# Kernel tuning notes

Hardware: AMD Instinct MI355X
Metric: run time of the kernel (lower is better)

The kernel has to match this reference:

```python
import jax, jax.numpy as jnp
import numpy as np


def setup_inputs() -> dict:
    key = jax.random.key(0)
    k0, k1, k2, k3 = jax.random.split(key, 4)
    B, H, W, C = 2, 128, 128, 512
    N_SPIX = 256  # (H/8)*(W/8) superpixels on an 8-px grid
    x = jax.random.normal(k0, (B, H, W, C), jnp.float32)
    sims = jax.random.uniform(k1, (B, H, W, 9), jnp.float32)
    sinds = jax.random.randint(k2, (B, H, W, 9), 0, N_SPIX, jnp.int32)
    W_qk = jax.random.normal(k3, (C, 2 * C), jnp.float32) * 0.02
    b_qk = jnp.zeros((2 * C,), jnp.float32)
    return {"x": x, "sims": sims, "sinds": sinds, "W_qk": W_qk, "b_qk": b_qk,
            "kernel_size": 7, "num_heads": 4}


def reference(x, sims, sinds, W_qk, b_qk, kernel_size, num_heads):
    """Soft-neighborhood superpixel attention scores.

    attn[b,g,si,h,w,ki] = <q[b,g,h,w], k[b,g,hj,wj]> + log p_j(s)
    where (hj,wj) is the ki-th pixel of the clamped (NATTEN-style) KxK window
    around (h,w), s = sinds[b,h,w,si] is the si-th neighboring-superpixel id
    of pixel (h,w), and p_j(s) = sum_m sims[b,hj,wj,m] * [sinds[b,hj,wj,m]==s]
    (the soft probability that key pixel j belongs to superpixel s; entries
    where s is not among j's 9 neighbor superpixels stay at -inf, matching
    the -inf-initialized attn buffer of the CUDA kernel).
    """
    B, H, W, C = x.shape
    K = kernel_size
    hd = C // num_heads
    r = K // 2

    # qk projection -> (B, heads, H, W, hd) for q and k (permute(3,0,4,1,2,5))
    qk = (x @ W_qk + b_qk).reshape(B, H, W, 2, num_heads, hd)
    q = jnp.moveaxis(qk[:, :, :, 0], 3, 1)  # (B,HD,H,W,hd)
    k = jnp.moveaxis(qk[:, :, :, 1], 3, 1)

    # NATTEN clamped window starts
    hs = jnp.clip(jnp.arange(H) - r, 0, H - K)  # (H,)
    ws = jnp.clip(jnp.arange(W) - r, 0, W - K)  # (W,)
    s_i = sinds  # (B,H,W,9): superpixel ids of pixel i's 9 neighbors

    dots, logps = [], []
    for dh in range(K):
        hj = hs + dh  # (H,)
        for dw in range(K):
            wj = ws + dw  # (W,)
            # gather key/sims/sinds at window offset (dh,dw)
            k_off = k[:, :, hj[:, None], wj[None, :], :]        # (B,HD,H,W,hd)
            dots.append(jnp.einsum('bghwf,bghwf->bghw', q, k_off))
            sind_j = sinds[:, hj[:, None], wj[None, :], :]      # (B,H,W,9)
            sim_j = sims[:, hj[:, None], wj[None, :], :]        # (B,H,W,9)
            # p_j(s_i): match i's si-th superpixel against j's 9 ids
            match = sind_j[:, :, :, None, :] == s_i[:, :, :, :, None]  # (B,H,W,9si,9m)
            pj = jnp.sum(jnp.where(match, sim_j[:, :, :, None, :], 0.0), axis=-1)  # (B,H,W,9)
            logps.append(jnp.where(pj > 0, jnp.log(jnp.maximum(pj, 1e-30)), -jnp.inf))

    dots = jnp.stack(dots, axis=-1)            # (B,HD,H,W,K*K)
    logp = jnp.stack(logps, axis=-1)           # (B,H,W,9,K*K)
    logp = jnp.moveaxis(logp, 3, 1)            # (B,9,H,W,K*K)
    attn = dots[:, :, None] + logp[:, None]    # (B,HD,9,H,W,K*K)
    return attn
```

## Files before the change

kernel.cpp:

```cpp
#include <hip/hip_runtime.h>
#include <hip/hip_bf16.h>
#include <math.h>

#define BATCH 2
#define HH 128
#define WW 128
#define CC 512
#define NH 4
#define HD 128
#define KS 7
#define RR 3
#define KK2 49
#define NSI 9

#define GM (BATCH*HH*WW)
#define GK CC
#define GN (2*CC)

#define NEG_HUGE (-1.0e30f)

typedef __attribute__((ext_vector_type(8))) short bf16x8;
typedef __attribute__((ext_vector_type(4))) float f32x4;

__device__ __forceinline__ float sout(float v) {
    return fminf(fmaxf(v, -3.0e38f), 3.0e38f);
}
__device__ __forceinline__ float bflo(unsigned int u) {
    return __builtin_bit_cast(float, u << 16);
}
__device__ __forceinline__ float bfhi(unsigned int u) {
    return __builtin_bit_cast(float, u & 0xffff0000u);
}
__device__ __forceinline__ unsigned short f2bf(float f) {
    unsigned int u = __builtin_bit_cast(unsigned int, f);
    u += 0x7fffu + ((u >> 16) & 1u);
    return (unsigned short)(u >> 16);
}

__device__ __forceinline__ void gl_lds16(const unsigned short* g, unsigned short* l) {
    __builtin_amdgcn_global_load_lds(
        (const __attribute__((address_space(1))) unsigned int*)g,
        (__attribute__((address_space(3))) unsigned int*)l, 16, 0, 0);
}

__global__ __launch_bounds__(256) void xcast(const float* __restrict__ x,
                                             unsigned short* __restrict__ xb) {
    int t = blockIdx.x * 256 + threadIdx.x;
    const float4* s = (const float4*)(x + (size_t)t * 8);
    float4 v0 = s[0], v1 = s[1];
    bf16x8 pk;
    pk[0] = (short)f2bf(v0.x); pk[1] = (short)f2bf(v0.y);
    pk[2] = (short)f2bf(v0.z); pk[3] = (short)f2bf(v0.w);
    pk[4] = (short)f2bf(v1.x); pk[5] = (short)f2bf(v1.y);
    pk[6] = (short)f2bf(v1.z); pk[7] = (short)f2bf(v1.w);
    *(bf16x8*)(xb + (size_t)t * 8) = pk;
}

__global__ __launch_bounds__(256) void wtrans(const float* __restrict__ W,
                                              unsigned short* __restrict__ Wt) {
    int t = blockIdx.x * 256 + threadIdx.x;
    int n = t >> 9, k = t & 511;
    Wt[(size_t)n * GK + k] = f2bf(W[(size_t)k * GN + n]);
}

#define TBM 128
#define TBN 128
#define TBK 64

__global__ __launch_bounds__(256, 3) void qk_gemm_async(
        const unsigned short* __restrict__ xb,
        const unsigned short* __restrict__ Wt,
        const float* __restrict__ bias,
        unsigned short* __restrict__ Cout)
{
    __shared__ unsigned short As[TBM * TBK];
    __shared__ unsigned short Bs[TBN * TBK];

    const int n0 = blockIdx.x * TBN;
    const int m0 = blockIdx.y * TBM;
    const int tid = threadIdx.x;
    const int lane = tid & 63;
    const int wid = tid >> 6;
    const int wr = wid >> 1, wc = wid & 1;

    f32x4 acc[4][4];
#pragma unroll
    for (int i = 0; i < 4; ++i)
#pragma unroll
        for (int j = 0; j < 4; ++j) acc[i][j] = (f32x4){0.f, 0.f, 0.f, 0.f};

    const int srow = lane >> 3;
    const int scol = (lane & 7) * 8;

    for (int k0 = 0; k0 < GK; k0 += TBK) {
#pragma unroll
        for (int i = 0; i < 4; ++i) {
            int chunk = wid * 4 + i;
            int row = chunk * 8 + srow;
            gl_lds16(xb + (size_t)(m0 + row) * GK + k0 + scol, &As[chunk * 512]);
            gl_lds16(Wt + (size_t)(n0 + row) * GK + k0 + scol, &Bs[chunk * 512]);
        }
        __syncthreads();

#pragma unroll
        for (int ks = 0; ks < 2; ++ks) {
            const int koff = ks * 32 + (lane >> 4) * 8;
            bf16x8 af[4], bfr[4];
#pragma unroll
            for (int i = 0; i < 4; ++i)
                af[i] = *(const bf16x8*)&As[(wr * 64 + i * 16 + (lane & 15)) * TBK + koff];
#pragma unroll
            for (int j = 0; j < 4; ++j)
                bfr[j] = *(const bf16x8*)&Bs[(wc * 64 + j * 16 + (lane & 15)) * TBK + koff];
#pragma unroll
            for (int i = 0; i < 4; ++i)
#pragma unroll
                for (int j = 0; j < 4; ++j)
                    acc[i][j] = __builtin_amdgcn_mfma_f32_16x16x32_bf16(
                        af[i], bfr[j], acc[i][j], 0, 0, 0);
        }
        __syncthreads();
    }

    const int colbase = n0 + wc * 64;
    float bias4[4];
#pragma unroll
    for (int j = 0; j < 4; ++j) bias4[j] = bias[colbase + j * 16 + (lane & 15)];
#pragma unroll
    for (int i = 0; i < 4; ++i)
#pragma unroll
        for (int j = 0; j < 4; ++j)
#pragma unroll
            for (int r = 0; r < 4; ++r) {
                int row = m0 + wr * 64 + i * 16 + (lane >> 4) * 4 + r;
                int col = colbase + j * 16 + (lane & 15);
                Cout[(size_t)row * GN + col] = f2bf(acc[i][j][r] + bias4[j]);
            }
}

#define LDAB 72

__global__ __launch_bounds__(256) void qk_gemm_conv(
        const float* __restrict__ X,
        const unsigned short* __restrict__ Wt,
        const float* __restrict__ bias,
        unsigned short* __restrict__ Cout)
{
    __shared__ unsigned short As[TBM][LDAB];
    __shared__ unsigned short Bs[TBN][LDAB];

    const int m0 = blockIdx.x * TBM;
    const int n0 = blockIdx.y * TBN;
    const int tid = threadIdx.x;
    const int lane = tid & 63;
    const int wid = tid >> 6;
    const int wr = wid >> 1, wc = wid & 1;

    f32x4 acc[4][4];
#pragma unroll
    for (int i = 0; i < 4; ++i)
#pragma unroll
        for (int j = 0; j < 4; ++j) acc[i][j] = (f32x4){0.f, 0.f, 0.f, 0.f};

    const int srow = tid >> 1;
    const int shalf = (tid & 1) * 32;

    for (int k0 = 0; k0 < GK; k0 += TBK) {
        {
            const float* srcA = X + (size_t)(m0 + srow) * GK + k0 + shalf;
#pragma unroll
            for (int i = 0; i < 4; ++i) {
                float4 v0 = ((const float4*)srcA)[i * 2];
                float4 v1 = ((const float4*)srcA)[i * 2 + 1];
                bf16x8 pk;
                pk[0] = (short)f2bf(v0.x); pk[1] = (short)f2bf(v0.y);
                pk[2] = (short)f2bf(v0.z); pk[3] = (short)f2bf(v0.w);
                pk[4] = (short)f2bf(v1.x); pk[5] = (short)f2bf(v1.y);
                pk[6] = (short)f2bf(v1.z); pk[7] = (short)f2bf(v1.w);
                *(bf16x8*)&As[srow][shalf + i * 8] = pk;
            }
        }
        {
            const unsigned short* srcB = Wt + (size_t)(n0 + srow) * GK + k0 + shalf;
#pragma unroll
            for (int i = 0; i < 4; ++i)
                *(uint4*)&Bs[srow][shalf + i * 8] = ((const uint4*)srcB)[i];
        }
        __syncthreads();

#pragma unroll
        for (int ks = 0; ks < 2; ++ks) {
            const int koff = ks * 32 + (lane >> 4) * 8;
            bf16x8 af[4], bfr[4];
#pragma unroll
            for (int i = 0; i < 4; ++i)
                af[i] = *(const bf16x8*)&As[wr * 64 + i * 16 + (lane & 15)][koff];
#pragma unroll
            for (int j = 0; j < 4; ++j)
                bfr[j] = *(const bf16x8*)&Bs[wc * 64 + j * 16 + (lane & 15)][koff];
#pragma unroll
            for (int i = 0; i < 4; ++i)
#pragma unroll
                for (int j = 0; j < 4; ++j)
                    acc[i][j] = __builtin_amdgcn_mfma_f32_16x16x32_bf16(
                        af[i], bfr[j], acc[i][j], 0, 0, 0);
        }
        __syncthreads();
    }

    const int colbase = n0 + wc * 64;
    float bias4[4];
#pragma unroll
    for (int j = 0; j < 4; ++j) bias4[j] = bias[colbase + j * 16 + (lane & 15)];
#pragma unroll
    for (int i = 0; i < 4; ++i)
#pragma unroll
        for (int j = 0; j < 4; ++j)
#pragma unroll
            for (int r = 0; r < 4; ++r) {
                int row = m0 + wr * 64 + i * 16 + (lane >> 4) * 4 + r;
                int col = colbase + j * 16 + (lane & 15);
                Cout[(size_t)row * GN + col] = f2bf(acc[i][j][r] + bias4[j]);
            }
}

#define HALO 14
#define LQK 136
#define LSS 212
#define NIT 13
#define NITEMS (64*KK2)

__global__ __launch_bounds__(256, 2) void attn_mfma(
        const unsigned short* __restrict__ qk,
        const float* __restrict__ sims,
        const int*   __restrict__ sinds,
        float* __restrict__ out)
{
    __shared__ __align__(16) unsigned char smem[208 * LQK * 2];
    unsigned short* Ks = (unsigned short*)smem;
    float* Ss = (float*)smem;

    const int tw = blockIdx.x, th = blockIdx.y, b = blockIdx.z;
    const int tid = threadIdx.x;
    const int lane = tid & 63;
    const int wm = tid >> 6;

    const int h0 = th * 8, w0 = tw * 8;
    const int hb = min(max(h0 - RR, 0), HH - KS);
    const int wb = min(max(w0 - RR, 0), WW - KS);

    unsigned int koff32[NIT];
    int jjv[NIT], ccv[NIT];
#pragma unroll
    for (int p = 0; p < NIT; ++p) {
        int o = tid + p * 256;
        int jj = o >> 4, c = o & 15;
        int jr = min(jj, HALO * HALO - 1);
        int hj = min(hb + jr / HALO, HH - 1);
        int wj = min(wb + jr % HALO, WW - 1);
        koff32[p] = (unsigned int)((((b * HH + hj) * WW + wj) * GN + CC + c * 8) * 2);
        jjv[p] = jj; ccv[p] = c;
    }

    const int pl_q = wm * 16 + (lane & 15);
    const size_t qrow = ((size_t)(b * HH + h0 + (pl_q >> 3)) * WW + w0 + (pl_q & 7)) * GN;
    const int kof8 = (lane >> 4) * 8;

    uint4 kbuf[NIT];
#pragma unroll
    for (int p = 0; p < NIT; ++p)
        kbuf[p] = *(const uint4*)((const char*)qk + koff32[p]);

    float dacc[NIT][NH];

#pragma unroll
    for (int g = 0; g < NH; ++g) {
        bf16x8 aq[4];
#pragma unroll
        for (int ks = 0; ks < 4; ++ks)
            aq[ks] = *(const bf16x8*)(qk + qrow + g * HD + ks * 32 + kof8);

#pragma unroll
        for (int p = 0; p < NIT; ++p)
            *(uint4*)&Ks[jjv[p] * LQK + ccv[p] * 8] = kbuf[p];
        __syncthreads();

        if (g < NH - 1) {
#pragma unroll
            for (int p = 0; p < NIT; ++p)
                kbuf[p] = *(const uint4*)((const char*)qk + koff32[p] + (g + 1) * 256);
        }

        __builtin_amdgcn_s_setprio(1);
        f32x4 svals[NIT];
#pragma unroll
        for (int nt = 0; nt < NIT; ++nt) {
            f32x4 sacc = (f32x4){0.f, 0.f, 0.f, 0.f};
#pragma unroll
            for (int ks = 0; ks < 4; ++ks) {
                bf16x8 bk = *(const bf16x8*)&Ks[(nt * 16 + (lane & 15)) * LQK + ks * 32 + kof8];
                sacc = __builtin_amdgcn_mfma_f32_16x16x32_bf16(aq[ks], bk, sacc, 0, 0, 0);
            }
            svals[nt] = sacc;
        }
        __builtin_amdgcn_s_setprio(0);
        __syncthreads();

#pragma unroll
        for (int nt = 0; nt < NIT; ++nt)
#pragma unroll
            for (int r = 0; r < 4; ++r) {
                int qr = wm * 16 + (lane >> 4) * 4 + r;
                Ss[qr * LSS + nt * 16 + (lane & 15)] = svals[nt][r];
            }
        __syncthreads();

#pragma unroll
        for (int r = 0; r < NIT; ++r) {
            int it = tid + r * 256;
            if (it < NITEMS) {
                int pl = it / KK2, ki = it % KK2;
                int h = h0 + (pl >> 3), w = w0 + (pl & 7);
                int dh = ki / KS, dw = ki % KS;
                int hj = min(max(h - RR, 0), HH - KS) + dh;
                int wj = min(max(w - RR, 0), WW - KS) + dw;
                int j = (hj - hb) * HALO + (wj - wb);
                dacc[r][g] = Ss[pl * LSS + j];
            }
        }
        __syncthreads();
    }

    const size_t plane = (size_t)HH * WW * KK2;
#pragma unroll
    for (int r = 0; r < NIT; ++r) {
        int it = tid + r * 256;
        if (it < NITEMS) {
            int pl = it / KK2, ki = it % KK2;
            int h = h0 + (pl >> 3), w = w0 + (pl & 7);
            int dh = ki / KS, dw = ki % KS;
            int hj = min(max(h - RR, 0), HH - KS) + dh;
            int wj = min(max(w - RR, 0), WW - KS) + dw;
            int pix = (b * HH + h) * WW + w;
            int pj  = (b * HH + hj) * WW + wj;

            int sid[NSI], sjd[NSI]; float sjm[NSI];
            const int*   sip = sinds + (size_t)pix * NSI;
            const int*   sjp = sinds + (size_t)pj * NSI;
            const float* smp = sims + (size_t)pj * NSI;
#pragma unroll
            for (int m = 0; m < NSI; ++m) { sid[m] = sip[m]; sjd[m] = sjp[m]; sjm[m] = smp[m]; }

            float lp[NSI];
#pragma unroll
            for (int si = 0; si < NSI; ++si) {
                float p = 0.f;
#pragma unroll
                for (int m = 0; m < NSI; ++m) p += (sjd[m] == sid[si]) ? sjm[m] : 0.f;
                lp[si] = (p > 0.f) ? __logf(fmaxf(p, 1e-30f)) : NEG_HUGE;
            }

            size_t inner = (size_t)(h * WW + w) * KK2 + ki;
#pragma unroll
            for (int g = 0; g < NH; ++g)
#pragma unroll
                for (int si = 0; si < NSI; ++si)
                    out[((size_t)((b * NH + g) * NSI + si)) * plane + inner] =
                        sout(dacc[r][g] + lp[si]);
        }
    }
}

#define FT 8
#define FH 14
#define FNP (FT*FT)
#define FNJ (FH*FH)
#define FDH 64
#define KPAD 68
#define FNITEM (FNP*KK2)
#define FNR 13

__global__ __launch_bounds__(256) void fused_attn(
        const float* __restrict__ x, const float* __restrict__ sims,
        const int* __restrict__ sinds, const float* __restrict__ Wm,
        const float* __restrict__ bias, float* __restrict__ out)
{
    __shared__ unsigned short kt[FNJ][KPAD];
    __shared__ unsigned short qt[FNP][KPAD];

    const int tw = blockIdx.x, th = blockIdx.y;
    const int b = blockIdx.z >> 2, g = blockIdx.z & 3;
    const int tid = threadIdx.x;
    const int hb = min(max(th * FT - RR, 0), HH - KS);
    const int wb = min(max(tw * FT - RR, 0), WW - KS);

    float dacc[FNR];
#pragma unroll
    for (int r = 0; r < FNR; ++r) dacc[r] = 0.f;

    for (int ph = 0; ph < 2; ++ph) {
        const int kcol0 = CC + g * HD + ph * FDH;
        const int qcol0 = g * HD + ph * FDH;

        for (int o = tid; o < FNJ * FDH; o += 256) {
            int j = o >> 6, dd = o & 63;
            int hj = min(hb + j / FH, HH - 1), wj = min(wb + j % FH, WW - 1);
            const float* xr = x + ((size_t)(b * HH + hj) * WW + wj) * CC;
            int col = kcol0 + dd;
            float acc = bias[col];
            for (int c = 0; c < CC; c += 4) {
                float4 xv = *(const float4*)(xr + c);
                acc += xv.x * Wm[(size_t)c * GN + col]
                     + xv.y * Wm[(size_t)(c + 1) * GN + col]
                     + xv.z * Wm[(size_t)(c + 2) * GN + col]
                     + xv.w * Wm[(size_t)(c + 3) * GN + col];
            }
            kt[j][dd] = f2bf(acc);
        }
        for (int o = tid; o < FNP * FDH; o += 256) {
            int i = o >> 6, dd = o & 63;
            int h = th * FT + (i >> 3), w = tw * FT + (i & 7);
            const float* xr = x + ((size_t)(b * HH + h) * WW + w) * CC;
            int col = qcol0 + dd;
            float acc = bias[col];
            for (int c = 0; c < CC; c += 4) {
                float4 xv = *(const float4*)(xr + c);
                acc += xv.x * Wm[(size_t)c * GN + col]
                     + xv.y * Wm[(size_t)(c + 1) * GN + col]
                     + xv.z * Wm[(size_t)(c + 2) * GN + col]
                     + xv.w * Wm[(size_t)(c + 3) * GN + col];
            }
            qt[i][dd] = f2bf(acc);
        }
        __syncthreads();

#pragma unroll
        for (int r = 0; r < FNR; ++r) {
            int it = tid + r * 256;
            if (it < FNITEM) {
                int pl = it / KK2, ki = it % KK2;
                int h = th * FT + (pl >> 3), w = tw * FT + (pl & 7);
                int dh = ki / KS, dw = ki % KS;
                int hj = min(max(h - RR, 0), HH - KS) + dh;
                int wj = min(max(w - RR, 0), WW - KS) + dw;
                int j = (hj - hb) * FH + (wj - wb);
                const unsigned int* qr = (const unsigned int*)&qt[pl][0];
                const unsigned int* kr = (const unsigned int*)&kt[j][0];
                float a = 0.f;
#pragma unroll 8
                for (int d = 0; d < FDH / 2; ++d) {
                    unsigned int qv = qr[d], kv = kr[d];
                    a += bflo(qv) * bflo(kv) + bfhi(qv) * bfhi(kv);
                }
                dacc[r] += a;
            }
        }
        __syncthreads();
    }

    const size_t plane = (size_t)HH * WW * KK2;
#pragma unroll
    for (int r = 0; r < FNR; ++r) {
        int it = tid + r * 256;
        if (it < FNITEM) {
            int pl = it / KK2, ki = it % KK2;
            int h = th * FT + (pl >> 3), w = tw * FT + (pl & 7);
            int dh = ki / KS, dw = ki % KS;
            int hj = min(max(h - RR, 0), HH - KS) + dh;
            int wj = min(max(w - RR, 0), WW - KS) + dw;
            int pix = (b * HH + h) * WW + w;
            int pj  = (b * HH + hj) * WW + wj;

            int sid[NSI], sjd[NSI]; float sjm[NSI];
            const int*   sip = sinds + (size_t)pix * NSI;
            const int*   sjp = sinds + (size_t)pj * NSI;
            const float* smp = sims + (size_t)pj * NSI;
#pragma unroll
            for (int m = 0; m < NSI; ++m) { sid[m] = sip[m]; sjd[m] = sjp[m]; sjm[m] = smp[m]; }

            const size_t inner = (size_t)(h * WW + w) * KK2 + ki;
#pragma unroll
            for (int si = 0; si < NSI; ++si) {
                float p = 0.f;
#pragma unroll
                for (int m = 0; m < NSI; ++m) p += (sjd[m] == sid[si]) ? sjm[m] : 0.f;
                float lp = (p > 0.f) ? __logf(fmaxf(p, 1e-30f)) : NEG_HUGE;
                out[((size_t)((b * NH + g) * NSI + si)) * plane + inner] =
                    sout(dacc[r] + lp);
            }
        }
    }
}

extern "C" void kernel_launch(void* const* d_in, const int* in_sizes, int n_in,
                              void* d_out, int out_size, void* d_ws, size_t ws_size,
                              hipStream_t stream) {
    const float* x     = (const float*)d_in[0];
    const float* sims  = (const float*)d_in[1];
    const int*   sinds = (const int*)d_in[2];
    const float* W_qk  = (const float*)d_in[3];
    const float* b_qk  = (const float*)d_in[4];
    float* out = (float*)d_out;

    const size_t qk_bytes = (size_t)GM * GN * sizeof(unsigned short);
    const size_t wt_bytes = (size_t)GN * GK * sizeof(unsigned short);
    const size_t xb_bytes = (size_t)GM * GK * sizeof(unsigned short);

    dim3 agrid(WW / 8, HH / 8, BATCH);

    if (ws_size >= qk_bytes + wt_bytes + xb_bytes) {
        unsigned short* qk = (unsigned short*)d_ws;
        unsigned short* Wt = (unsigned short*)((char*)d_ws + qk_bytes);
        unsigned short* xb = (unsigned short*)((char*)d_ws + qk_bytes + wt_bytes);

        wtrans<<<(GK * GN) / 256, 256, 0, stream>>>(W_qk, Wt);
        xcast<<<(GM * GK) / (256 * 8), 256, 0, stream>>>(x, xb);
        dim3 ggrid(GN / TBN, GM / TBM);
        qk_gemm_async<<<ggrid, 256, 0, stream>>>(xb, Wt, b_qk, qk);
        attn_mfma<<<agrid, 256, 0, stream>>>(qk, sims, sinds, out);
    } else if (ws_size >= qk_bytes + wt_bytes) {
        unsigned short* qk = (unsigned short*)d_ws;
        unsigned short* Wt = (unsigned short*)((char*)d_ws + qk_bytes);

        wtrans<<<(GK * GN) / 256, 256, 0, stream>>>(W_qk, Wt);
        dim3 ggrid(GM / TBM, GN / TBN);
        qk_gemm_conv<<<ggrid, 256, 0, stream>>>(x, Wt, b_qk, qk);
        attn_mfma<<<agrid, 256, 0, stream>>>(qk, sims, sinds, out);
    } else {
        dim3 fgrid(WW / FT, HH / FT, BATCH * NH);
        fused_attn<<<fgrid, 256, 0, stream>>>(x, sims, sinds, W_qk, b_qk, out);
    }
}
```

Baseline: 195.0 us.

## Shrink attn_mfma registers and LDS, swizzle block order, emit output per head

Restructures the attention kernel so each head's outputs are written inside the head loop. This drops the dacc[13][4] array and the register prefetch of the next head's K tile. LDS is cut (row count clamped to 196, LSS changed to 209) and launch bounds are raised to 3 blocks per CU for higher occupancy. A 1D grid with a bid&7 swizzle spreads the 512 tiles across XCDs. The trade-off is that the sims/sinds loads and the logp computation now run once per head instead of once, and the overlap of K loads with compute is lost.

```diff
diff --git a/kernel.cpp b/kernel.cpp
--- a/kernel.cpp
+++ b/kernel.cpp
@@ -225,22 +225,28 @@
 }
 
 #define HALO 14
+#define NKROW 196
 #define LQK 136
-#define LSS 212
+#define LSS 209
 #define NIT 13
 #define NITEMS (64*KK2)
 
-__global__ __launch_bounds__(256, 2) void attn_mfma(
+__global__ __launch_bounds__(256, 3) void attn_mfma(
         const unsigned short* __restrict__ qk,
         const float* __restrict__ sims,
         const int*   __restrict__ sinds,
         float* __restrict__ out)
 {
-    __shared__ __align__(16) unsigned char smem[208 * LQK * 2];
+    __shared__ __align__(16) unsigned char smem[64 * LSS * 4];
     unsigned short* Ks = (unsigned short*)smem;
     float* Ss = (float*)smem;
 
-    const int tw = blockIdx.x, th = blockIdx.y, b = blockIdx.z;
+    const int bid = blockIdx.x;
+    const int spatial = (bid & 7) * 64 + (bid >> 3);
+    const int tw = spatial & 15;
+    const int th = (spatial >> 4) & 15;
+    const int b  = spatial >> 8;
+
     const int tid = threadIdx.x;
     const int lane = tid & 63;
     const int wm = tid >> 6;
@@ -249,56 +255,49 @@
     const int hb = min(max(h0 - RR, 0), HH - KS);
     const int wb = min(max(w0 - RR, 0), WW - KS);
 
-    unsigned int koff32[NIT];
-    int jjv[NIT], ccv[NIT];
+    unsigned int koff[NIT];
+    int jrow[NIT];
 #pragma unroll
     for (int p = 0; p < NIT; ++p) {
         int o = tid + p * 256;
         int jj = o >> 4, c = o & 15;
-        int jr = min(jj, HALO * HALO - 1);
+        int jr = min(jj, NKROW - 1);
         int hj = min(hb + jr / HALO, HH - 1);
         int wj = min(wb + jr % HALO, WW - 1);
-        koff32[p] = (unsigned int)((((b * HH + hj) * WW + wj) * GN + CC + c * 8) * 2);
-        jjv[p] = jj; ccv[p] = c;
+        koff[p] = (unsigned int)(((((b * HH + hj) * WW + wj) * GN) + CC + c * 8) * 2);
+        jrow[p] = jr;
     }
 
     const int pl_q = wm * 16 + (lane & 15);
     const size_t qrow = ((size_t)(b * HH + h0 + (pl_q >> 3)) * WW + w0 + (pl_q & 7)) * GN;
     const int kof8 = (lane >> 4) * 8;
-
-    uint4 kbuf[NIT];
-#pragma unroll
-    for (int p = 0; p < NIT; ++p)
-        kbuf[p] = *(const uint4*)((const char*)qk + koff32[p]);
-
-    float dacc[NIT][NH];
-
-#pragma unroll
+    const size_t plane = (size_t)HH * WW * KK2;
+
     for (int g = 0; g < NH; ++g) {
+        uint4 kb[NIT];
+#pragma unroll
+        for (int p = 0; p < NIT; ++p)
+            kb[p] = *(const uint4*)((const char*)qk + koff[p] + g * 256);
         bf16x8 aq[4];
 #pragma unroll
         for (int ks = 0; ks < 4; ++ks)
             aq[ks] = *(const bf16x8*)(qk + qrow + g * HD + ks * 32 + kof8);
-
-#pragma unroll
-        for (int p = 0; p < NIT; ++p)
-            *(uint4*)&Ks[jjv[p] * LQK + ccv[p] * 8] = kbuf[p];
-        __syncthreads();
-
-        if (g < NH - 1) {
-#pragma unroll
-            for (int p = 0; p < NIT; ++p)
-                kbuf[p] = *(const uint4*)((const char*)qk + koff32[p] + (g + 1) * 256);
-        }
+#pragma unroll
+        for (int p = 0; p < NIT; ++p) {
+            int c = (tid + p * 256) & 15;
+            *(uint4*)&Ks[jrow[p] * LQK + c * 8] = kb[p];
+        }
+        __syncthreads();
 
         __builtin_amdgcn_s_setprio(1);
         f32x4 svals[NIT];
 #pragma unroll
         for (int nt = 0; nt < NIT; ++nt) {
+            int rB = min(nt * 16 + (lane & 15), NKROW - 1);
             f32x4 sacc = (f32x4){0.f, 0.f, 0.f, 0.f};
 #pragma unroll
             for (int ks = 0; ks < 4; ++ks) {
-                bf16x8 bk = *(const bf16x8*)&Ks[(nt * 16 + (lane & 15)) * LQK + ks * 32 + kof8];
+                bf16x8 bk = *(const bf16x8*)&Ks[rB * LQK + ks * 32 + kof8];
                 sacc = __builtin_amdgcn_mfma_f32_16x16x32_bf16(aq[ks], bk, sacc, 0, 0, 0);
             }
             svals[nt] = sacc;
@@ -316,8 +315,8 @@
         __syncthreads();
 
 #pragma unroll
-        for (int r = 0; r < NIT; ++r) {
-            int it = tid + r * 256;
+        for (int rr = 0; rr < NIT; ++rr) {
+            int it = tid + rr * 256;
             if (it < NITEMS) {
                 int pl = it / KK2, ki = it % KK2;
                 int h = h0 + (pl >> 3), w = w0 + (pl & 7);
@@ -325,49 +324,30 @@
                 int hj = min(max(h - RR, 0), HH - KS) + dh;
                 int wj = min(max(w - RR, 0), WW - KS) + dw;
                 int j = (hj - hb) * HALO + (wj - wb);
-                dacc[r][g] = Ss[pl * LSS + j];
-            }
-        }
-        __syncthreads();
-    }
-
-    const size_t plane = (size_t)HH * WW * KK2;
-#pragma unroll
-    for (int r = 0; r < NIT; ++r) {
-        int it = tid + r * 256;
-        if (it < NITEMS) {
-            int pl = it / KK2, ki = it % KK2;
-            int h = h0 + (pl >> 3), w = w0 + (pl & 7);
-            int dh = ki / KS, dw = ki % KS;
-            int hj = min(max(h - RR, 0), HH - KS) + dh;
-            int wj = min(max(w - RR, 0), WW - KS) + dw;
-            int pix = (b * HH + h) * WW + w;
-            int pj  = (b * HH + hj) * WW + wj;
-
-            int sid[NSI], sjd[NSI]; float sjm[NSI];
-            const int*   sip = sinds + (size_t)pix * NSI;
-            const int*   sjp = sinds + (size_t)pj * NSI;
-            const float* smp = sims + (size_t)pj * NSI;
-#pragma unroll
-            for (int m = 0; m < NSI; ++m) { sid[m] = sip[m]; sjd[m] = sjp[m]; sjm[m] = smp[m]; }
-
-            float lp[NSI];
-#pragma unroll
-            for (int si = 0; si < NSI; ++si) {
-                float p = 0.f;
-#pragma unroll
-                for (int m = 0; m < NSI; ++m) p += (sjd[m] == sid[si]) ? sjm[m] : 0.f;
-                lp[si] = (p > 0.f) ? __logf(fmaxf(p, 1e-30f)) : NEG_HUGE;
-            }
-
-            size_t inner = (size_t)(h * WW + w) * KK2 + ki;
-#pragma unroll
-            for (int g = 0; g < NH; ++g)
-#pragma unroll
-                for (int si = 0; si < NSI; ++si)
+                float dot = Ss[pl * LSS + j];
+                int pix = (b * HH + h) * WW + w;
+                int pj  = (b * HH + hj) * WW + wj;
+
+                int sid[NSI], sjd[NSI]; float sjm[NSI];
+                const int*   sip = sinds + (size_t)pix * NSI;
+                const int*   sjp = sinds + (size_t)pj * NSI;
+                const float* smp = sims + (size_t)pj * NSI;
+#pragma unroll
+                for (int m = 0; m < NSI; ++m) { sid[m] = sip[m]; sjd[m] = sjp[m]; sjm[m] = smp[m]; }
+
+                size_t inner = (size_t)(h * WW + w) * KK2 + ki;
+#pragma unroll
+                for (int si = 0; si < NSI; ++si) {
+                    float p = 0.f;
+#pragma unroll
+                    for (int m = 0; m < NSI; ++m) p += (sjd[m] == sid[si]) ? sjm[m] : 0.f;
+                    float lp = (p > 0.f) ? __logf(fmaxf(p, 1e-30f)) : NEG_HUGE;
                     out[((size_t)((b * NH + g) * NSI + si)) * plane + inner] =
-                        sout(dacc[r][g] + lp[si]);
-        }
+                        sout(dot + lp);
+                }
+            }
+        }
+        __syncthreads();
     }
 }
 
@@ -506,8 +486,6 @@
     const size_t wt_bytes = (size_t)GN * GK * sizeof(unsigned short);
     const size_t xb_bytes = (size_t)GM * GK * sizeof(unsigned short);
 
-    dim3 agrid(WW / 8, HH / 8, BATCH);
-
     if (ws_size >= qk_bytes + wt_bytes + xb_bytes) {
         unsigned short* qk = (unsigned short*)d_ws;
         unsigned short* Wt = (unsigned short*)((char*)d_ws + qk_bytes);
@@ -517,7 +495,7 @@
         xcast<<<(GM * GK) / (256 * 8), 256, 0, stream>>>(x, xb);
         dim3 ggrid(GN / TBN, GM / TBM);
         qk_gemm_async<<<ggrid, 256, 0, stream>>>(xb, Wt, b_qk, qk);
-        attn_mfma<<<agrid, 256, 0, stream>>>(qk, sims, sinds, out);
+        attn_mfma<<<512, 256, 0, stream>>>(qk, sims, sinds, out);
     } else if (ws_size >= qk_bytes + wt_bytes) {
         unsigned short* qk = (unsigned short*)d_ws;
         unsigned short* Wt = (unsigned short*)((char*)d_ws + qk_bytes);
@@ -525,7 +503,7 @@
         wtrans<<<(GK * GN) / 256, 256, 0, stream>>>(W_qk, Wt);
         dim3 ggrid(GM / TBM, GN / TBN);
         qk_gemm_conv<<<ggrid, 256, 0, stream>>>(x, Wt, b_qk, qk);
-        attn_mfma<<<agrid, 256, 0, stream>>>(qk, sims, sinds, out);
+        attn_mfma<<<512, 256, 0, stream>>>(qk, sims, sinds, out);
     } else {
         dim3 fgrid(WW / FT, HH / FT, BATCH * NH);
         fused_attn<<<fgrid, 256, 0, stream>>>(x, sims, sinds, W_qk, b_qk, out);
```

Measured after the change: 251.7 us. +29.1%, slower.
